# Kernel tuning notes

Hardware: AMD Instinct MI355X
Metric: run time of the kernel (lower is better)

## Reference

```python
import jax, jax.numpy as jnp
import numpy as np
import math

H, DH, DP, DE = 8, 16, 128, 32   # heads, dim_head, dim_p_embd, dim_embd
M = 64                            # number of random features
EPS = 1e-4                        # softmax_kernel eps
LN_EPS = 1e-5


def gelu(x):
    # exact tanh-approx gelu used in the source
    return 0.5 * x * (1.0 + jnp.tanh(math.sqrt(2.0 / math.pi) * (x + 0.044715 * x ** 3)))


def layernorm(x, w, b):
    mu = x.mean(-1, keepdims=True)
    var = ((x - mu) ** 2).mean(-1, keepdims=True)
    return (x - mu) / jnp.sqrt(var + LN_EPS) * w + b


def softmax_kernel(data, proj, is_query):
    # FAVOR+ positive random-feature softmax kernel
    dn = data.shape[-1] ** -0.25
    ratio = proj.shape[0] ** -0.5
    dash = jnp.einsum('bhnd,md->bhnm', dn * data, proj)
    diag = (data ** 2).sum(-1, keepdims=True) * (0.5 * dn * dn)
    unnorm = ratio * jnp.exp(dash - diag)
    if is_query:
        mx = jax.lax.stop_gradient(jnp.max(dash, axis=-1, keepdims=True))
    else:
        mx = jax.lax.stop_gradient(jnp.max(dash, axis=(-1, -2), keepdims=True))
    return unnorm * jnp.exp(-mx) + ratio * EPS, unnorm


def linear_attention(q, k, v):
    k_sum = k.sum(-2)                                        # (b,h,m)
    d_inv = 1.0 / jnp.einsum('bhnm,bhm->bhn', q, k_sum)
    ctx = jnp.einsum('bhnm,bhne->bhme', k, v)                # (b,h,m,d)
    return jnp.einsum('bhme,bhnm,bhn->bhne', ctx, q, d_inv)


def heads(t):
    b, n, _ = t.shape
    return t.reshape(b, n, H, DH).transpose(0, 2, 1, 3)      # b n (h d) -> b h n d


def setup_inputs() -> dict:
    key = jax.random.key(0)
    ks = jax.random.split(key, 12)
    B, NCTX, NQ = 16, 3200, 3072
    std = 0.02
    return {
        'x': jax.random.normal(ks[0], (B, NCTX, DE), jnp.float32),
        'y': jax.random.normal(ks[1], (2, B, NQ, DP), jnp.float32),
        'proj': jax.random.normal(ks[2], (M, DH), jnp.float32),
        'ln1_w': jnp.ones((DP,), jnp.float32), 'ln1_b': jnp.zeros((DP,), jnp.float32),
        'ln2_w': jnp.ones((DE,), jnp.float32), 'ln2_b': jnp.zeros((DE,), jnp.float32),
        'ln4_w': jnp.ones((DP,), jnp.float32), 'ln4_b': jnp.zeros((DP,), jnp.float32),
        'fc_w': std * jax.random.normal(ks[3], (DP, DP), jnp.float32),
        'fc_b': jnp.zeros((DP,), jnp.float32),
        'pr_w': std * jax.random.normal(ks[4], (DP, DP), jnp.float32),
        'pr_b': jnp.zeros((DP,), jnp.float32),
        'wq': std * jax.random.normal(ks[5], (DP, DP), jnp.float32),
        'wk': std * jax.random.normal(ks[6], (DP, DE), jnp.float32),
        'wv': std * jax.random.normal(ks[7], (DP, DE), jnp.float32),
        'wo': std * jax.random.normal(ks[8], (DP, DP), jnp.float32),
        'wo_b': jnp.zeros((DP,), jnp.float32),
    }


def reference(x, y, proj, ln1_w, ln1_b, ln2_w, ln2_b, ln4_w, ln4_b,
              fc_w, fc_b, pr_w, pr_b, wq, wk, wv, wo, wo_b):
    # --- MLP(dim_p_embd) pre-attention residual (Conv1D: x @ W + b) ---
    h = gelu(layernorm(y, ln4_w, ln4_b) @ fc_w + fc_b)
    y1 = h @ pr_w + pr_b + y                                 # (2,B,NQ,DP)

    xq = layernorm(y1, ln1_w, ln1_b)
    ctx = layernorm(x, ln2_w, ln2_b)
    B, NCTX, _ = x.shape
    NQ = y.shape[2]

    q = heads(xq.reshape(-1, NQ, DP) @ wq.T)                 # (2B,H,NQ,DH)
    k = heads(ctx @ wk.T)                                    # (B,H,NCTX,DH)
    v = heads(ctx @ wv.T)

    # temporal split: doubles the batch, drops first/last s tokens
    s = NCTX * 2 // 50
    k2 = jnp.concatenate([k[None, :, :, :-s], k[None, :, :, s:]], 0).reshape(2 * B, H, NCTX - s, DH)
    v2 = jnp.concatenate([v[None, :, :, :-s], v[None, :, :, s:]], 0).reshape(2 * B, H, NCTX - s, DH)

    qf, q_unnorm = softmax_kernel(q, proj, True)
    kf, k_unnorm = softmax_kernel(k2, proj, False)
    out = linear_attention(qf, kf, v2)                       # (2B,H,NQ,DH)

    out = out.transpose(0, 2, 1, 3).reshape(2 * B, NQ, DP) @ wo.T + wo_b
    y_out = y1 + out.reshape(y.shape)
    return y_out, q_unnorm[:, :, None], k_unnorm[:, :, None]
```

## Files before the change

### kernel.cpp

```cpp
#include <hip/hip_runtime.h>
#include <math.h>

constexpr int cH = 8;
constexpr int cDP = 128;
constexpr int cM = 64;
constexpr int cB = 16;
constexpr int cNCTX = 3200;
constexpr int cNQ = 3072;
constexpr int cSHIFT = 128;
constexpr int ROWS_Q = 2 * cB * cNQ;
constexpr int ROWS_KV = cB * cNCTX;
constexpr float cRATIO = 0.125f;
constexpr float cEPST = 0.125e-4f;
constexpr float cLNEPS = 1e-5f;

typedef float f32x4 __attribute__((ext_vector_type(4)));
typedef short short8 __attribute__((ext_vector_type(8)));
typedef _Float16 half2 __attribute__((ext_vector_type(2)));

#define MFMA16x16(a, b, c) __builtin_amdgcn_mfma_f32_16x16x32_bf16((a), (b), (c), 0, 0, 0)

__device__ __forceinline__ float wmax64(float v) {
#pragma unroll
  for (int o = 32; o; o >>= 1) v = fmaxf(v, __shfl_xor(v, o));
  return v;
}
__device__ __forceinline__ float wsum64(float v) {
#pragma unroll
  for (int o = 32; o; o >>= 1) v += __shfl_xor(v, o);
  return v;
}
__device__ __forceinline__ float gelu_f(float x) {
  return 0.5f * x * (1.0f + tanhf(0.79788456080286536f * (x + 0.044715f * x * x * x)));
}
__device__ __forceinline__ unsigned int bf16r(float f) {
  unsigned int x = __float_as_uint(f);
  return (x + 0x7fffu + ((x >> 16) & 1u)) >> 16;
}
__device__ __forceinline__ unsigned int f16r(float f) {
  _Float16 hh = (_Float16)f;
  unsigned short u;
  __builtin_memcpy(&u, &hh, 2);
  return (unsigned int)u;
}
__device__ __forceinline__ void cvt8(uint4 u, float f[8]) {
  f[0] = __uint_as_float(u.x << 16);
  f[1] = __uint_as_float(u.x & 0xffff0000u);
  f[2] = __uint_as_float(u.y << 16);
  f[3] = __uint_as_float(u.y & 0xffff0000u);
  f[4] = __uint_as_float(u.z << 16);
  f[5] = __uint_as_float(u.z & 0xffff0000u);
  f[6] = __uint_as_float(u.w << 16);
  f[7] = __uint_as_float(u.w & 0xffff0000u);
}
__device__ __forceinline__ int swz(int row, int k) {
  return row * 128 + ((((k >> 3) ^ (row & 15)) << 3) | (k & 7));
}

__global__ __launch_bounds__(256) void k0_prep(
    const float* __restrict__ fcw, const float* __restrict__ prw,
    const float* __restrict__ wq, const float* __restrict__ wo,
    unsigned short* __restrict__ fcT, unsigned short* __restrict__ prT,
    unsigned short* __restrict__ wqT, unsigned short* __restrict__ woT) {
  const int mat = blockIdx.x;
  const float* src = mat == 0 ? fcw : mat == 1 ? prw : mat == 2 ? wq : wo;
  unsigned short* dst = mat == 0 ? fcT : mat == 1 ? prT : mat == 2 ? wqT : woT;
  const bool tr = (mat < 2);
  for (int i = threadIdx.x; i < 16384; i += 256) {
    int n = i >> 7, k = i & 127;
    float f = tr ? src[k * 128 + n] : src[i];
    dst[swz(n, k)] = (unsigned short)(mat == 2 ? f16r(f) : bf16r(f));
  }
}

__global__ __launch_bounds__(256, 2) void k1_mlp(
    const float* __restrict__ y,
    const float* __restrict__ ln4w, const float* __restrict__ ln4b,
    const unsigned short* __restrict__ fcT, const float* __restrict__ fcb,
    const unsigned short* __restrict__ prT, const float* __restrict__ prb,
    float* __restrict__ y1) {
  __shared__ unsigned short wfc[16384];
  __shared__ unsigned short wpr[16384];
  __shared__ unsigned short xb[4096];
  __shared__ unsigned short hb[4096];
  const int tid = threadIdx.x;
  {
    const uint4* s1 = (const uint4*)fcT; uint4* d1 = (uint4*)wfc;
    const uint4* s2 = (const uint4*)prT; uint4* d2 = (uint4*)wpr;
    for (int i = tid; i < 2048; i += 256) { d1[i] = s1[i]; d2[i] = s2[i]; }
  }
  const int lane = tid & 63, wv = tid >> 6;
  const int lrow = tid >> 3, lsub = tid & 7;
  const int colbase = wv * 32;
  float fb[2], pb[2];
#pragma unroll
  for (int ct = 0; ct < 2; ++ct) {
    int col = colbase + ct * 16 + (lane & 15);
    fb[ct] = fcb[col];
    pb[ct] = prb[col];
  }
  float lw[16], lb[16];
  *(float4*)&lw[0] = *(const float4*)(ln4w + lsub * 16 + 0);
  *(float4*)&lw[4] = *(const float4*)(ln4w + lsub * 16 + 4);
  *(float4*)&lw[8] = *(const float4*)(ln4w + lsub * 16 + 8);
  *(float4*)&lw[12] = *(const float4*)(ln4w + lsub * 16 + 12);
  *(float4*)&lb[0] = *(const float4*)(ln4b + lsub * 16 + 0);
  *(float4*)&lb[4] = *(const float4*)(ln4b + lsub * 16 + 4);
  *(float4*)&lb[8] = *(const float4*)(ln4b + lsub * 16 + 8);
  *(float4*)&lb[12] = *(const float4*)(ln4b + lsub * 16 + 12);
  uint4* xb4 = (uint4*)xb;
  __syncthreads();

  for (int g = blockIdx.x; g < ROWS_Q / 32; g += gridDim.x) {
    const int r0 = g * 32;
    {
      const float* yr = y + (size_t)(r0 + lrow) * 128 + lsub * 16;
      float v[16];
      *(float4*)&v[0] = *(const float4*)(yr + 0);
      *(float4*)&v[4] = *(const float4*)(yr + 4);
      *(float4*)&v[8] = *(const float4*)(yr + 8);
      *(float4*)&v[12] = *(const float4*)(yr + 12);
      float s = 0.f, q = 0.f;
#pragma unroll
      for (int j = 0; j < 16; ++j) { s += v[j]; q += v[j] * v[j]; }
#pragma unroll
      for (int o = 1; o <= 4; o <<= 1) { s += __shfl_xor(s, o); q += __shfl_xor(q, o); }
      float mu = s * (1.0f / 128.0f);
      float rs = rsqrtf(q * (1.0f / 128.0f) - mu * mu + cLNEPS);
      unsigned int us[8];
#pragma unroll
      for (int j = 0; j < 8; ++j) {
        float f0 = (v[2 * j] - mu) * rs * lw[2 * j] + lb[2 * j];
        float f1 = (v[2 * j + 1] - mu) * rs * lw[2 * j + 1] + lb[2 * j + 1];
        us[j] = bf16r(f0) | (bf16r(f1) << 16);
      }
      int s0 = (lsub * 2) ^ (lrow & 15), s1 = (lsub * 2 + 1) ^ (lrow & 15);
      xb4[lrow * 16 + s0] = make_uint4(us[0], us[1], us[2], us[3]);
      xb4[lrow * 16 + s1] = make_uint4(us[4], us[5], us[6], us[7]);
    }
    __syncthreads();
    {
      f32x4 acc[2][2] = {{{0.f,0.f,0.f,0.f},{0.f,0.f,0.f,0.f}},
                         {{0.f,0.f,0.f,0.f},{0.f,0.f,0.f,0.f}}};
#pragma unroll
      for (int kc = 0; kc < 4; ++kc) {
        short8 af[2], bfv[2];
#pragma unroll
        for (int rt = 0; rt < 2; ++rt) {
          int row = rt * 16 + (lane & 15);
          int slot = ((lane >> 4) + kc * 4) ^ (row & 15);
          af[rt] = *(const short8*)&xb[row * 128 + slot * 8];
        }
#pragma unroll
        for (int ct = 0; ct < 2; ++ct) {
          int col = colbase + ct * 16 + (lane & 15);
          int slot = ((lane >> 4) + kc * 4) ^ (col & 15);
          bfv[ct] = *(const short8*)&wfc[col * 128 + slot * 8];
        }
#pragma unroll
        for (int rt = 0; rt < 2; ++rt)
#pragma unroll
          for (int ct = 0; ct < 2; ++ct)
            acc[rt][ct] = MFMA16x16(af[rt], bfv[ct], acc[rt][ct]);
      }
#pragma unroll
      for (int rt = 0; rt < 2; ++rt)
#pragma unroll
        for (int ct = 0; ct < 2; ++ct) {
          int col = colbase + ct * 16 + (lane & 15);
#pragma unroll
          for (int reg = 0; reg < 4; ++reg) {
            int row = rt * 16 + (lane >> 4) * 4 + reg;
            hb[swz(row, col)] = (unsigned short)bf16r(gelu_f(acc[rt][ct][reg] + fb[ct]));
          }
        }
    }
    __syncthreads();
    {
      f32x4 a2[2][2] = {{{0.f,0.f,0.f,0.f},{0.f,0.f,0.f,0.f}},
                        {{0.f,0.f,0.f,0.f},{0.f,0.f,0.f,0.f}}};
#pragma unroll
      for (int kc = 0; kc < 4; ++kc) {
        short8 af[2], bfv[2];
#pragma unroll
        for (int rt = 0; rt < 2; ++rt) {
          int row = rt * 16 + (lane & 15);
          int slot = ((lane >> 4) + kc * 4) ^ (row & 15);
          af[rt] = *(const short8*)&hb[row * 128 + slot * 8];
        }
#pragma unroll
        for (int ct = 0; ct < 2; ++ct) {
          int col = colbase + ct * 16 + (lane & 15);
          int slot = ((lane >> 4) + kc * 4) ^ (col & 15);
          bfv[ct] = *(const short8*)&wpr[col * 128 + slot * 8];
        }
#pragma unroll
        for (int rt = 0; rt < 2; ++rt)
#pragma unroll
          for (int ct = 0; ct < 2; ++ct)
            a2[rt][ct] = MFMA16x16(af[rt], bfv[ct], a2[rt][ct]);
      }
#pragma unroll
      for (int rt = 0; rt < 2; ++rt)
#pragma unroll
        for (int ct = 0; ct < 2; ++ct) {
          int col = colbase + ct * 16 + (lane & 15);
#pragma unroll
          for (int reg = 0; reg < 4; ++reg) {
            int row = rt * 16 + (lane >> 4) * 4 + reg;
            size_t o = (size_t)(r0 + row) * 128 + col;
            y1[o] = a2[rt][ct][reg] + pb[ct] + y[o];
          }
        }
    }
    __syncthreads();
  }
}

__global__ __launch_bounds__(512) void k2_kv(
    const float* __restrict__ x,
    const float* __restrict__ ln2w, const float* __restrict__ ln2b,
    const float* __restrict__ wkw, const float* __restrict__ wvw,
    float* __restrict__ kbuf, float* __restrict__ vbuf) {
  __shared__ float wkT[32 * cDP];
  __shared__ float wvT[32 * cDP];
  __shared__ float xbs[16][32];
  const int tid = threadIdx.x;
  for (int i = tid; i < 32 * cDP; i += 512) {
    int j = i >> 5, d = i & 31;
    wkT[d * cDP + j] = wkw[i];
    wvT[d * cDP + j] = wvw[i];
  }
  const int dl = tid & 31, rl = tid >> 5;
  const int col = tid & 127, rh = tid >> 7;
  const float l2w = ln2w[dl], l2b = ln2b[dl];
  __syncthreads();
  for (int g = blockIdx.x; g < ROWS_KV / 16; g += gridDim.x) {
    const int r0 = g * 16;
    __syncthreads();
    {
      float v = x[(size_t)(r0 + rl) * 32 + dl];
      float s = v, q = v * v;
#pragma unroll
      for (int o = 16; o; o >>= 1) { s += __shfl_xor(s, o); q += __shfl_xor(q, o); }
      float mu = s * (1.0f / 32.0f);
      float var = q * (1.0f / 32.0f) - mu * mu;
      xbs[rl][dl] = (v - mu) * rsqrtf(var + cLNEPS) * l2w + l2b;
    }
    __syncthreads();
    float ak0 = 0, ak1 = 0, ak2 = 0, ak3 = 0, av0 = 0, av1 = 0, av2 = 0, av3 = 0;
    for (int d = 0; d < 32; d += 4) {
      float4 v0 = *(const float4*)&xbs[rh * 4 + 0][d];
      float4 v1 = *(const float4*)&xbs[rh * 4 + 1][d];
      float4 v2 = *(const float4*)&xbs[rh * 4 + 2][d];
      float4 v3 = *(const float4*)&xbs[rh * 4 + 3][d];
      float k0 = wkT[(d + 0) * cDP + col], k1 = wkT[(d + 1) * cDP + col];
      float k2 = wkT[(d + 2) * cDP + col], k3 = wkT[(d + 3) * cDP + col];
      float u0 = wvT[(d + 0) * cDP + col], u1 = wvT[(d + 1) * cDP + col];
      float u2 = wvT[(d + 2) * cDP + col], u3 = wvT[(d + 3) * cDP + col];
      ak0 += v0.x * k0 + v0.y * k1 + v0.z * k2 + v0.w * k3;
      ak1 += v1.x * k0 + v1.y * k1 + v1.z * k2 + v1.w * k3;
      ak2 += v2.x * k0 + v2.y * k1 + v2.z * k2 + v2.w * k3;
      ak3 += v3.x * k0 + v3.y * k1 + v3.z * k2 + v3.w * k3;
      av0 += v0.x * u0 + v0.y * u1 + v0.z * u2 + v0.w * u3;
      av1 += v1.x * u0 + v1.y * u1 + v1.z * u2 + v1.w * u3;
      av2 += v2.x * u0 + v2.y * u1 + v2.z * u2 + v2.w * u3;
      av3 += v3.x * u0 + v3.y * u1 + v3.z * u2 + v3.w * u3;
    }
    kbuf[(size_t)(r0 + rh * 4 + 0) * cDP + col] = ak0;
    kbuf[(size_t)(r0 + rh * 4 + 1) * cDP + col] = ak1;
    kbuf[(size_t)(r0 + rh * 4 + 2) * cDP + col] = ak2;
    kbuf[(size_t)(r0 + rh * 4 + 3) * cDP + col] = ak3;
    vbuf[(size_t)(r0 + rh * 4 + 0) * cDP + col] = av0;
    vbuf[(size_t)(r0 + rh * 4 + 1) * cDP + col] = av1;
    vbuf[(size_t)(r0 + rh * 4 + 2) * cDP + col] = av2;
    vbuf[(size_t)(r0 + rh * 4 + 3) * cDP + col] = av3;
  }
}

__global__ __launch_bounds__(512) void k4_kun(
    const float* __restrict__ kbuf, const float* __restrict__ proj,
    float* __restrict__ k_un, float* __restrict__ tmax) {
  __shared__ float kb[16][cDP];
  const int tid = threadIdx.x;
  const int m = tid & 63, h = tid >> 6, lane = tid & 63;
  float pr[16];
#pragma unroll
  for (int d = 0; d < 16; ++d) pr[d] = proj[m * 16 + d];
  for (int g = blockIdx.x; g < ROWS_KV / 16; g += gridDim.x) {
    const int r0 = g * 16;
    __syncthreads();
    for (int i = tid; i < 16 * cDP; i += 512)
      kb[i >> 7][i & 127] = kbuf[(size_t)(r0 + (i >> 7)) * cDP + (i & 127)];
    __syncthreads();
    const int b = r0 / cNCTX;
    for (int r4 = 0; r4 < 16; r4 += 4) {
      float dashv[4];
#pragma unroll
      for (int j = 0; j < 4; ++j) {
        int r = r4 + j;
        float4 q0 = *(const float4*)&kb[r][h * 16 + 0];
        float4 q1 = *(const float4*)&kb[r][h * 16 + 4];
        float4 q2 = *(const float4*)&kb[r][h * 16 + 8];
        float4 q3 = *(const float4*)&kb[r][h * 16 + 12];
        float dash = q0.x * pr[0] + q0.y * pr[1] + q0.z * pr[2] + q0.w * pr[3]
                   + q1.x * pr[4] + q1.y * pr[5] + q1.z * pr[6] + q1.w * pr[7]
                   + q2.x * pr[8] + q2.y * pr[9] + q2.z * pr[10] + q2.w * pr[11]
                   + q3.x * pr[12] + q3.y * pr[13] + q3.z * pr[14] + q3.w * pr[15];
        dash *= 0.5f;
        float ss = q0.x * q0.x + q0.y * q0.y + q0.z * q0.z + q0.w * q0.w
                 + q1.x * q1.x + q1.y * q1.y + q1.z * q1.z + q1.w * q1.w
                 + q2.x * q2.x + q2.y * q2.y + q2.z * q2.z + q2.w * q2.w
                 + q3.x * q3.x + q3.y * q3.y + q3.z * q3.z + q3.w * q3.w;
        dashv[j] = dash;
        float un = cRATIO * __expf(dash - 0.125f * ss);
        int t = r0 + r - b * cNCTX;
        if (t < cNQ)
          k_un[((size_t)(b * cH + h) * cNQ + t) * cM + m] = un;
        if (t >= cSHIFT)
          k_un[((size_t)((b + cB) * cH + h) * cNQ + (t - cSHIFT)) * cM + m] = un;
      }
      float m0 = dashv[0], m1 = dashv[1], m2 = dashv[2], m3 = dashv[3];
#pragma unroll
      for (int o = 32; o; o >>= 1) {
        float t0 = __shfl_xor(m0, o), t1 = __shfl_xor(m1, o);
        float t2 = __shfl_xor(m2, o), t3 = __shfl_xor(m3, o);
        m0 = fmaxf(m0, t0); m1 = fmaxf(m1, t1);
        m2 = fmaxf(m2, t2); m3 = fmaxf(m3, t3);
      }
      if (lane == 0) {
        int tb = (b * cH + h) * cNCTX + (r0 - b * cNCTX) + r4;
        tmax[tb + 0] = m0;
        tmax[tb + 1] = m1;
        tmax[tb + 2] = m2;
        tmax[tb + 3] = m3;
      }
    }
  }
}

__global__ __launch_bounds__(256) void k4b_mxk(
    const float* __restrict__ tmax, float* __restrict__ mxk) {
  const int bh = blockIdx.x;
  const int tid = threadIdx.x;
  float m0 = -1e30f, m1 = -1e30f;
  for (int t = tid; t < cNCTX; t += 256) {
    float v = tmax[bh * cNCTX + t];
    if (t < cNQ) m0 = fmaxf(m0, v);
    if (t >= cSHIFT) m1 = fmaxf(m1, v);
  }
  __shared__ float s0[256], s1[256];
  s0[tid] = m0; s1[tid] = m1;
  __syncthreads();
  for (int s = 128; s; s >>= 1) {
    if (tid < s) { s0[tid] = fmaxf(s0[tid], s0[tid + s]); s1[tid] = fmaxf(s1[tid], s1[tid + s]); }
    __syncthreads();
  }
  if (tid == 0) { mxk[bh] = s0[0]; mxk[bh + 128] = s1[0]; }
}

__global__ __launch_bounds__(256) void k5a_ctx(
    const float* __restrict__ k_un, const float* __restrict__ vbuf,
    const float* __restrict__ mxk,
    float* __restrict__ part_c, float* __restrict__ part_k) {
  const int bbh = blockIdx.x;
  const int ch = blockIdx.y;
  const int bb = bbh >> 3, h = bbh & 7;
  const int b = bb & 15, toff = (bb >> 4) * cSHIFT;
  const float ek = expf(-mxk[bbh]);
  const int tid = threadIdx.x, m = tid & 63, eq = tid >> 6;
  __shared__ float ub[64][64];
  __shared__ float vb[64][16];
  float c0 = 0, c1 = 0, c2 = 0, c3 = 0, ks = 0;
  const int nb = ch * 512;
  for (int n0 = nb; n0 < nb + 512; n0 += 64) {
    for (int i = tid; i < 64 * 64; i += 256)
      ub[i >> 6][i & 63] = k_un[((size_t)bbh * cNQ + n0 + (i >> 6)) * cM + (i & 63)];
    for (int i = tid; i < 64 * 16; i += 256)
      vb[i >> 4][i & 15] = vbuf[((size_t)(b * cNCTX) + toff + n0 + (i >> 4)) * cDP + h * 16 + (i & 15)];
    __syncthreads();
#pragma unroll 4
    for (int nn = 0; nn < 64; ++nn) {
      float kf = ub[nn][m] * ek + cEPST;
      ks += kf;
      float4 vv = *(const float4*)&vb[nn][eq * 4];
      c0 += kf * vv.x; c1 += kf * vv.y; c2 += kf * vv.z; c3 += kf * vv.w;
    }
    __syncthreads();
  }
  size_t po = (size_t)ch * 256 + bbh;
  part_c[po * 1024 + m * 16 + eq * 4 + 0] = c0;
  part_c[po * 1024 + m * 16 + eq * 4 + 1] = c1;
  part_c[po * 1024 + m * 16 + eq * 4 + 2] = c2;
  part_c[po * 1024 + m * 16 + eq * 4 + 3] = c3;
  if (eq == 0) part_k[po * 64 + m] = ks;
}

__global__ __launch_bounds__(256) void k5a2_red(
    const float* __restrict__ part_c, const float* __restrict__ part_k,
    float* __restrict__ ctx2, float* __restrict__ ksum) {
  const int bbh = blockIdx.x;
  const int tid = threadIdx.x;
  for (int i = tid; i < 1024; i += 256) {
    float s = 0;
#pragma unroll
    for (int ch = 0; ch < 6; ++ch) s += part_c[((size_t)ch * 256 + bbh) * 1024 + i];
    ctx2[bbh * 1024 + i] = s;
  }
  if (tid < 64) {
    float s = 0;
#pragma unroll
    for (int ch = 0; ch < 6; ++ch) s += part_k[((size_t)ch * 256 + bbh) * 64 + tid];
    ksum[bbh * cM + tid] = s;
  }
}

__global__ __launch_bounds__(512, 4) void kq_fused2(
    const float* __restrict__ y1,
    const float* __restrict__ ln1w, const float* __restrict__ ln1b,
    const unsigned short* __restrict__ wqT, const float* __restrict__ proj,
    const float* __restrict__ ctx2, const float* __restrict__ ksum,
    float* __restrict__ q_un, float* __restrict__ attn) {
  __shared__ unsigned short wqs[128 * 128];
  __shared__ unsigned short xb[32 * 128];
  __shared__ float qb[32][132];
  __shared__ unsigned short qfl[8][16][72];
  __shared__ float dvv[8][16];
  const int tid = threadIdx.x;
  const int bb = blockIdx.y;
  {
    const uint4* s1 = (const uint4*)wqT; uint4* d1 = (uint4*)wqs;
    for (int i = tid; i < 2048; i += 512) d1[i] = s1[i];
  }
  const int lane = tid & 63, wvid = tid >> 6;
  const int lrow = tid >> 4, c8 = tid & 15;
  const int cx = tid & 31, ry2 = tid >> 5;
  const int m = lane;
  const int h = wvid;
  float pr[16];
#pragma unroll
  for (int d = 0; d < 16; ++d) pr[d] = proj[m * 16 + d];
  short8 bfr[2], bks[2];
  {
    const float* cp = ctx2 + (size_t)(bb * cH + h) * 1024;
    const float* kp = ksum + (size_t)(bb * cH + h) * cM;
#pragma unroll
    for (int kh = 0; kh < 2; ++kh) {
      short8 bfv, bkv;
#pragma unroll
      for (int j = 0; j < 8; ++j) {
        int mm = kh * 32 + (lane >> 4) * 8 + j;
        ((unsigned short*)&bfv)[j] = (unsigned short)bf16r(cp[mm * 16 + (lane & 15)]);
        ((unsigned short*)&bkv)[j] =
            ((lane & 15) == 0) ? (unsigned short)bf16r(kp[mm]) : (unsigned short)0;
      }
      bfr[kh] = bfv;
      bks[kh] = bkv;
    }
  }
  float lw[8], lb[8];
  *(float4*)&lw[0] = *(const float4*)(ln1w + c8 * 8 + 0);
  *(float4*)&lw[4] = *(const float4*)(ln1w + c8 * 8 + 4);
  *(float4*)&lb[0] = *(const float4*)(ln1b + c8 * 8 + 0);
  *(float4*)&lb[4] = *(const float4*)(ln1b + c8 * 8 + 4);
  uint4* xb4 = (uint4*)xb;
  const uint4* wq4 = (const uint4*)wqs;
  __syncthreads();

  for (int tile = blockIdx.x; tile < 96; tile += 16) {
    const int n0 = tile * 32;
    const size_t r0g = (size_t)bb * cNQ + n0;
    {
      const float* yr = y1 + (r0g + lrow) * 128 + c8 * 8;
      float v[8];
      *(float4*)&v[0] = *(const float4*)(yr + 0);
      *(float4*)&v[4] = *(const float4*)(yr + 4);
      float s = 0.f, q = 0.f;
#pragma unroll
      for (int j = 0; j < 8; ++j) { s += v[j]; q += v[j] * v[j]; }
#pragma unroll
      for (int o = 1; o <= 8; o <<= 1) { s += __shfl_xor(s, o); q += __shfl_xor(q, o); }
      float mu = s * (1.0f / 128.0f);
      float rs = rsqrtf(q * (1.0f / 128.0f) - mu * mu + cLNEPS);
      unsigned int us[4];
#pragma unroll
      for (int j = 0; j < 4; ++j) {
        float f0 = (v[2 * j] - mu) * rs * lw[2 * j] + lb[2 * j];
        float f1 = (v[2 * j + 1] - mu) * rs * lw[2 * j + 1] + lb[2 * j + 1];
        us[j] = f16r(f0) | (f16r(f1) << 16);
      }
      xb4[lrow * 16 + (c8 ^ (lrow & 15))] = make_uint4(us[0], us[1], us[2], us[3]);
    }
    __syncthreads();
    {
      float acc[2][4] = {};
#pragma unroll 2
      for (int kg = 0; kg < 16; ++kg) {
        uint4 xv[2], wv[4];
#pragma unroll
        for (int rr = 0; rr < 2; ++rr) {
          int r = ry2 * 2 + rr;
          xv[rr] = xb4[r * 16 + (kg ^ (r & 15))];
        }
#pragma unroll
        for (int cc = 0; cc < 4; ++cc) {
          int c = cx + 32 * cc;
          wv[cc] = wq4[c * 16 + (kg ^ (c & 15))];
        }
#pragma unroll
        for (int cc = 0; cc < 4; ++cc) {
          const half2* wh = (const half2*)&wv[cc];
#pragma unroll
          for (int rr = 0; rr < 2; ++rr) {
            const half2* xh = (const half2*)&xv[rr];
#pragma unroll
            for (int p = 0; p < 4; ++p)
              acc[rr][cc] = __builtin_amdgcn_fdot2(xh[p], wh[p], acc[rr][cc], false);
          }
        }
      }
#pragma unroll
      for (int rr = 0; rr < 2; ++rr)
#pragma unroll
        for (int cc = 0; cc < 4; ++cc)
          qb[ry2 * 2 + rr][cx + 32 * cc] = acc[rr][cc];
    }
    __syncthreads();
    float ssv;
    {
      int r = lane & 31;
      float4 s0 = *(const float4*)&qb[r][h * 16 + 0];
      float4 s1 = *(const float4*)&qb[r][h * 16 + 4];
      float4 s2 = *(const float4*)&qb[r][h * 16 + 8];
      float4 s3 = *(const float4*)&qb[r][h * 16 + 12];
      ssv = s0.x * s0.x + s0.y * s0.y + s0.z * s0.z + s0.w * s0.w
          + s1.x * s1.x + s1.y * s1.y + s1.z * s1.z + s1.w * s1.w
          + s2.x * s2.x + s2.y * s2.y + s2.z * s2.z + s2.w * s2.w
          + s3.x * s3.x + s3.y * s3.y + s3.z * s3.z + s3.w * s3.w;
    }
#pragma unroll
    for (int half = 0; half < 2; ++half) {
      for (int rr = 0; rr < 16; rr += 4) {
        float dashv[4], unv[4];
#pragma unroll
        for (int j = 0; j < 4; ++j) {
          int r = half * 16 + rr + j;
          float4 a0 = *(const float4*)&qb[r][h * 16 + 0];
          float4 a1 = *(const float4*)&qb[r][h * 16 + 4];
          float4 a2 = *(const float4*)&qb[r][h * 16 + 8];
          float4 a3 = *(const float4*)&qb[r][h * 16 + 12];
          float dash = a0.x * pr[0] + a0.y * pr[1] + a0.z * pr[2] + a0.w * pr[3]
                     + a1.x * pr[4] + a1.y * pr[5] + a1.z * pr[6] + a1.w * pr[7]
                     + a2.x * pr[8] + a2.y * pr[9] + a2.z * pr[10] + a2.w * pr[11]
                     + a3.x * pr[12] + a3.y * pr[13] + a3.z * pr[14] + a3.w * pr[15];
          dash *= 0.5f;
          dashv[j] = dash;
          float ss = __shfl(ssv, r);
          unv[j] = cRATIO * __expf(dash - 0.125f * ss);
          q_un[((size_t)(bb * cH + h) * cNQ + n0 + r) * cM + m] = unv[j];
        }
        float m0 = dashv[0], m1 = dashv[1], m2 = dashv[2], m3 = dashv[3];
#pragma unroll
        for (int o = 32; o; o >>= 1) {
          float t0 = __shfl_xor(m0, o), t1 = __shfl_xor(m1, o);
          float t2 = __shfl_xor(m2, o), t3 = __shfl_xor(m3, o);
          m0 = fmaxf(m0, t0); m1 = fmaxf(m1, t1);
          m2 = fmaxf(m2, t2); m3 = fmaxf(m3, t3);
        }
        qfl[wvid][rr + 0][lane] = (unsigned short)bf16r(unv[0] * __expf(-m0) + cEPST);
        qfl[wvid][rr + 1][lane] = (unsigned short)bf16r(unv[1] * __expf(-m1) + cEPST);
        qfl[wvid][rr + 2][lane] = (unsigned short)bf16r(unv[2] * __expf(-m2) + cEPST);
        qfl[wvid][rr + 3][lane] = (unsigned short)bf16r(unv[3] * __expf(-m3) + cEPST);
      }
      {
        const unsigned short* qp = &qfl[wvid][0][0];
        int ab = (lane & 15) * 72 + (lane >> 4) * 8;
        short8 a0 = *(const short8*)&qp[ab];
        short8 a1 = *(const short8*)&qp[ab + 32];
        f32x4 cd = {0.f, 0.f, 0.f, 0.f};
        cd = MFMA16x16(a0, bks[0], cd);
        cd = MFMA16x16(a1, bks[1], cd);
        if ((lane & 15) == 0) {
#pragma unroll
          for (int reg = 0; reg < 4; ++reg)
            dvv[wvid][(lane >> 4) * 4 + reg] = 1.0f / cd[reg];
        }
        f32x4 c = {0.f, 0.f, 0.f, 0.f};
        c = MFMA16x16(a0, bfr[0], c);
        c = MFMA16x16(a1, bfr[1], c);
#pragma unroll
        for (int reg = 0; reg < 4; ++reg) {
          int rloc = (lane >> 4) * 4 + reg;
          attn[(r0g + half * 16 + rloc) * cDP + h * 16 + (lane & 15)] =
              c[reg] * dvv[wvid][rloc];
        }
      }
    }
    __syncthreads();
  }
}

__global__ __launch_bounds__(256, 2) void k6_wo(
    const float* __restrict__ attn,
    const unsigned short* __restrict__ woT, const float* __restrict__ wob,
    const float* __restrict__ y1, float* __restrict__ yout) {
  __shared__ unsigned short wos[16384];
  __shared__ unsigned short xb[4096];
  const int tid = threadIdx.x;
  {
    const uint4* s1 = (const uint4*)woT; uint4* d1 = (uint4*)wos;
    for (int i = tid; i < 2048; i += 256) d1[i] = s1[i];
  }
  const int lane = tid & 63, wv = tid >> 6;
  const int lrow = tid >> 3, lsub = tid & 7;
  const int colbase = wv * 32;
  float wb[2];
#pragma unroll
  for (int ct = 0; ct < 2; ++ct) wb[ct] = wob[colbase + ct * 16 + (lane & 15)];
  uint4* xb4 = (uint4*)xb;
  __syncthreads();
  for (int g = blockIdx.x; g < ROWS_Q / 32; g += gridDim.x) {
    const int r0 = g * 32;
    {
      const float* ar = attn + (size_t)(r0 + lrow) * 128 + lsub * 16;
      float v[16];
      *(float4*)&v[0] = *(const float4*)(ar + 0);
      *(float4*)&v[4] = *(const float4*)(ar + 4);
      *(float4*)&v[8] = *(const float4*)(ar + 8);
      *(float4*)&v[12] = *(const float4*)(ar + 12);
      unsigned int us[8];
#pragma unroll
      for (int j = 0; j < 8; ++j)
        us[j] = bf16r(v[2 * j]) | (bf16r(v[2 * j + 1]) << 16);
      int s0 = (lsub * 2) ^ (lrow & 15), s1 = (lsub * 2 + 1) ^ (lrow & 15);
      xb4[lrow * 16 + s0] = make_uint4(us[0], us[1], us[2], us[3]);
      xb4[lrow * 16 + s1] = make_uint4(us[4], us[5], us[6], us[7]);
    }
    __syncthreads();
    {
      f32x4 acc[2][2] = {{{0.f,0.f,0.f,0.f},{0.f,0.f,0.f,0.f}},
                         {{0.f,0.f,0.f,0.f},{0.f,0.f,0.f,0.f}}};
#pragma unroll
      for (int kc = 0; kc < 4; ++kc) {
        short8 af[2], bfv[2];
#pragma unroll
        for (int rt = 0; rt < 2; ++rt) {
          int row = rt * 16 + (lane & 15);
          int slot = ((lane >> 4) + kc * 4) ^ (row & 15);
          af[rt] = *(const short8*)&xb[row * 128 + slot * 8];
        }
#pragma unroll
        for (int ct = 0; ct < 2; ++ct) {
          int col = colbase + ct * 16 + (lane & 15);
          int slot = ((lane >> 4) + kc * 4) ^ (col & 15);
          bfv[ct] = *(const short8*)&wos[col * 128 + slot * 8];
        }
#pragma unroll
        for (int rt = 0; rt < 2; ++rt)
#pragma unroll
          for (int ct = 0; ct < 2; ++ct)
            acc[rt][ct] = MFMA16x16(af[rt], bfv[ct], acc[rt][ct]);
      }
#pragma unroll
      for (int rt = 0; rt < 2; ++rt)
#pragma unroll
        for (int ct = 0; ct < 2; ++ct) {
          int col = colbase + ct * 16 + (lane & 15);
#pragma unroll
          for (int reg = 0; reg < 4; ++reg) {
            int row = rt * 16 + (lane >> 4) * 4 + reg;
            size_t o = (size_t)(r0 + row) * 128 + col;
            yout[o] = acc[rt][ct][reg] + wb[ct] + y1[o];
          }
        }
    }
    __syncthreads();
  }
}

extern "C" void kernel_launch(void* const* d_in, const int* in_sizes, int n_in,
                              void* d_out, int out_size, void* d_ws, size_t ws_size,
                              hipStream_t stream) {
  (void)in_sizes; (void)n_in; (void)out_size; (void)ws_size;
  const float* x = (const float*)d_in[0];
  const float* y = (const float*)d_in[1];
  const float* proj = (const float*)d_in[2];
  const float* ln1w = (const float*)d_in[3];
  const float* ln1b = (const float*)d_in[4];
  const float* ln2w = (const float*)d_in[5];
  const float* ln2b = (const float*)d_in[6];
  const float* ln4w = (const float*)d_in[7];
  const float* ln4b = (const float*)d_in[8];
  const float* fcw = (const float*)d_in[9];
  const float* fcb = (const float*)d_in[10];
  const float* prw = (const float*)d_in[11];
  const float* prb = (const float*)d_in[12];
  const float* wq = (const float*)d_in[13];
  const float* wk = (const float*)d_in[14];
  const float* wv = (const float*)d_in[15];
  const float* wo = (const float*)d_in[16];
  const float* wob = (const float*)d_in[17];

  float* out = (float*)d_out;
  float* q_un = out + 12582912;
  float* k_un = out + 62914560;

  float* ws = (float*)d_ws;
  float* y1 = ws;
  float* kbuf = ws + 12582912;
  float* vbuf = ws + 19136512;
  float* part_c = ws + 12582912;
  float* part_k = ws + 14155776;
  float* attn = ws + 12582912;
  float* tmax = ws + 26476544;
  float* mxk = ws + 26886144;
  float* ksum = ws + 26886400;
  float* ctx2 = ws + 26902784;
  unsigned short* fcT = (unsigned short*)(ws + 27164928);
  unsigned short* prT = fcT + 16384;
  unsigned short* wqT = prT + 16384;
  unsigned short* woT = wqT + 16384;

  k0_prep<<<dim3(4), dim3(256), 0, stream>>>(fcw, prw, wq, wo, fcT, prT, wqT, woT);
  k1_mlp<<<dim3(512), dim3(256), 0, stream>>>(y, ln4w, ln4b, fcT, fcb, prT, prb, y1);
  k2_kv<<<dim3(400), dim3(512), 0, stream>>>(x, ln2w, ln2b, wk, wv, kbuf, vbuf);
  k4_kun<<<dim3(400), dim3(512), 0, stream>>>(kbuf, proj, k_un, tmax);
  k4b_mxk<<<dim3(128), dim3(256), 0, stream>>>(tmax, mxk);
  k5a_ctx<<<dim3(256, 6), dim3(256), 0, stream>>>(k_un, vbuf, mxk, part_c, part_k);
  k5a2_red<<<dim3(256), dim3(256), 0, stream>>>(part_c, part_k, ctx2, ksum);
  kq_fused2<<<dim3(16, 32), dim3(512), 0, stream>>>(y1, ln1w, ln1b, wqT, proj,
                                                    ctx2, ksum, q_un, attn);
  k6_wo<<<dim3(512), dim3(256), 0, stream>>>(attn, woT, wob, y1, out);
}
```

Before: 398.3 us.

## Read GEMM weights from global/L2 instead of staging in LDS, raise occupancy

The MLP, Q-projection and output-projection kernels no longer copy the 128x128 bf16 weight matrices into shared memory. They read the B fragments directly from global memory, relying on L1/L2 caching. This frees LDS, and the launch bounds are raised to allow more resident blocks. The trade-off is that every K-chunk now issues global loads that may have higher latency than LDS reads.

```diff
diff --git a/kernel.cpp b/kernel.cpp
--- a/kernel.cpp
+++ b/kernel.cpp
@@ -42,16 +42,6 @@
   unsigned short u;
   __builtin_memcpy(&u, &hh, 2);
   return (unsigned int)u;
-}
-__device__ __forceinline__ void cvt8(uint4 u, float f[8]) {
-  f[0] = __uint_as_float(u.x << 16);
-  f[1] = __uint_as_float(u.x & 0xffff0000u);
-  f[2] = __uint_as_float(u.y << 16);
-  f[3] = __uint_as_float(u.y & 0xffff0000u);
-  f[4] = __uint_as_float(u.z << 16);
-  f[5] = __uint_as_float(u.z & 0xffff0000u);
-  f[6] = __uint_as_float(u.w << 16);
-  f[7] = __uint_as_float(u.w & 0xffff0000u);
 }
 __device__ __forceinline__ int swz(int row, int k) {
   return row * 128 + ((((k >> 3) ^ (row & 15)) << 3) | (k & 7));
@@ -73,22 +63,15 @@
   }
 }
 
-__global__ __launch_bounds__(256, 2) void k1_mlp(
+__global__ __launch_bounds__(256, 4) void k1_mlp(
     const float* __restrict__ y,
     const float* __restrict__ ln4w, const float* __restrict__ ln4b,
     const unsigned short* __restrict__ fcT, const float* __restrict__ fcb,
     const unsigned short* __restrict__ prT, const float* __restrict__ prb,
     float* __restrict__ y1) {
-  __shared__ unsigned short wfc[16384];
-  __shared__ unsigned short wpr[16384];
   __shared__ unsigned short xb[4096];
   __shared__ unsigned short hb[4096];
   const int tid = threadIdx.x;
-  {
-    const uint4* s1 = (const uint4*)fcT; uint4* d1 = (uint4*)wfc;
-    const uint4* s2 = (const uint4*)prT; uint4* d2 = (uint4*)wpr;
-    for (int i = tid; i < 2048; i += 256) { d1[i] = s1[i]; d2[i] = s2[i]; }
-  }
   const int lane = tid & 63, wv = tid >> 6;
   const int lrow = tid >> 3, lsub = tid & 7;
   const int colbase = wv * 32;
@@ -109,7 +92,6 @@
   *(float4*)&lb[8] = *(const float4*)(ln4b + lsub * 16 + 8);
   *(float4*)&lb[12] = *(const float4*)(ln4b + lsub * 16 + 12);
   uint4* xb4 = (uint4*)xb;
-  __syncthreads();
 
   for (int g = blockIdx.x; g < ROWS_Q / 32; g += gridDim.x) {
     const int r0 = g * 32;
@@ -155,7 +137,7 @@
         for (int ct = 0; ct < 2; ++ct) {
           int col = colbase + ct * 16 + (lane & 15);
           int slot = ((lane >> 4) + kc * 4) ^ (col & 15);
-          bfv[ct] = *(const short8*)&wfc[col * 128 + slot * 8];
+          bfv[ct] = *(const short8*)&fcT[col * 128 + slot * 8];
         }
 #pragma unroll
         for (int rt = 0; rt < 2; ++rt)
@@ -192,7 +174,7 @@
         for (int ct = 0; ct < 2; ++ct) {
           int col = colbase + ct * 16 + (lane & 15);
           int slot = ((lane >> 4) + kc * 4) ^ (col & 15);
-          bfv[ct] = *(const short8*)&wpr[col * 128 + slot * 8];
+          bfv[ct] = *(const short8*)&prT[col * 128 + slot * 8];
         }
 #pragma unroll
         for (int rt = 0; rt < 2; ++rt)
@@ -421,17 +403,12 @@
     const unsigned short* __restrict__ wqT, const float* __restrict__ proj,
     const float* __restrict__ ctx2, const float* __restrict__ ksum,
     float* __restrict__ q_un, float* __restrict__ attn) {
-  __shared__ unsigned short wqs[128 * 128];
   __shared__ unsigned short xb[32 * 128];
   __shared__ float qb[32][132];
   __shared__ unsigned short qfl[8][16][72];
   __shared__ float dvv[8][16];
   const int tid = threadIdx.x;
   const int bb = blockIdx.y;
-  {
-    const uint4* s1 = (const uint4*)wqT; uint4* d1 = (uint4*)wqs;
-    for (int i = tid; i < 2048; i += 512) d1[i] = s1[i];
-  }
   const int lane = tid & 63, wvid = tid >> 6;
   const int lrow = tid >> 4, c8 = tid & 15;
   const int cx = tid & 31, ry2 = tid >> 5;
@@ -464,8 +441,7 @@
   *(float4*)&lb[0] = *(const float4*)(ln1b + c8 * 8 + 0);
   *(float4*)&lb[4] = *(const float4*)(ln1b + c8 * 8 + 4);
   uint4* xb4 = (uint4*)xb;
-  const uint4* wq4 = (const uint4*)wqs;
-  __syncthreads();
+  const uint4* wq4 = (const uint4*)wqT;
 
   for (int tile = blockIdx.x; tile < 96; tile += 16) {
     const int n0 = tile * 32;
@@ -600,17 +576,12 @@
   }
 }
 
-__global__ __launch_bounds__(256, 2) void k6_wo(
+__global__ __launch_bounds__(256, 8) void k6_wo(
     const float* __restrict__ attn,
     const unsigned short* __restrict__ woT, const float* __restrict__ wob,
     const float* __restrict__ y1, float* __restrict__ yout) {
-  __shared__ unsigned short wos[16384];
   __shared__ unsigned short xb[4096];
   const int tid = threadIdx.x;
-  {
-    const uint4* s1 = (const uint4*)woT; uint4* d1 = (uint4*)wos;
-    for (int i = tid; i < 2048; i += 256) d1[i] = s1[i];
-  }
   const int lane = tid & 63, wv = tid >> 6;
   const int lrow = tid >> 3, lsub = tid & 7;
   const int colbase = wv * 32;
@@ -618,7 +589,6 @@
 #pragma unroll
   for (int ct = 0; ct < 2; ++ct) wb[ct] = wob[colbase + ct * 16 + (lane & 15)];
   uint4* xb4 = (uint4*)xb;
-  __syncthreads();
   for (int g = blockIdx.x; g < ROWS_Q / 32; g += gridDim.x) {
     const int r0 = g * 32;
     {
@@ -653,7 +623,7 @@
         for (int ct = 0; ct < 2; ++ct) {
           int col = colbase + ct * 16 + (lane & 15);
           int slot = ((lane >> 4) + kc * 4) ^ (col & 15);
-          bfv[ct] = *(const short8*)&wos[col * 128 + slot * 8];
+          bfv[ct] = *(const short8*)&woT[col * 128 + slot * 8];
         }
 #pragma unroll
         for (int rt = 0; rt < 2; ++rt)
```

Result: slower. 521.3 us (+30.9%).
